# Optimization experiments

Hardware: AMD Instinct MI355X
Metric: run time of the kernel (lower is better)

The kernel has to match this reference:

```python
import jax, jax.numpy as jnp
import numpy as np

B, N, H = 64, 1024, 64
ALPHA = 0.2  # leaky relu negative slope
NEG_BIG = -1.0e12


def setup_inputs() -> dict:
    key = jax.random.key(0)
    k1, k2, k3, k4, k5, k6 = jax.random.split(key, 6)
    inp = jax.random.normal(k1, (B, N, H), dtype=jnp.float32)
    inp_none = jax.random.normal(k2, (B, N, H), dtype=jnp.float32)
    A = (jax.random.uniform(k3, (B, N, N)) < 0.1).astype(jnp.float32)
    # per-sample [i, j] ranges, i <= j < N
    l = jnp.sort(jax.random.randint(k4, (B, 2), 0, N), axis=1)
    # xavier_uniform with gain=1.414 on shape (2H, 1)
    bound = 1.414 * np.sqrt(6.0 / (2 * H + 1))
    a_i = jax.random.uniform(k5, (2 * H, 1), minval=-bound, maxval=bound, dtype=jnp.float32)
    a_c = jax.random.uniform(k6, (2 * H, 1), minval=-bound, maxval=bound, dtype=jnp.float32)
    return {"inp": inp, "inp_none": inp_none, "A": A, "l": l, "a_i": a_i, "a_c": a_c}


def reference(inp, inp_none, A, l, a_i, a_c):
    h = inp.shape[-1]
    n = inp.shape[1]
    # additive-score halves: [B, N, 1]
    Wh1_i = inp_none @ a_i[:h]
    Wh2_i = inp @ a_i[h:]
    Wh1_c = inp @ a_c[:h]
    Wh2_c = inp @ a_c[h:]
    # vectorized replacement of the per-sample range overwrite loop:
    # rows in [l[b,0], l[b,1]) take the a_i branch
    pos = jnp.arange(n)[None, :, None]                       # [1, N, 1]
    in_range = (pos >= l[:, 0, None, None]) & (pos < l[:, 1, None, None])  # [B, N, 1]
    Wh1 = jnp.where(in_range, Wh1_i, Wh1_c)                  # [B, N, 1]
    Wh2 = jnp.where(in_range, Wh2_i, Wh2_c)                  # [B, N, 1]
    # e[b, p, q] = leakyrelu((Wh1[b,p] + Wh2[b,q]) * A[b,p,q])
    e = (Wh1 + jnp.swapaxes(Wh2, 1, 2)) * A                  # [B, N, N]
    e = jnp.where(e >= 0, e, ALPHA * e)
    attn = jnp.where(A > 0, e, NEG_BIG)
    attn = jax.nn.softmax(attn, axis=2)
    h_prime = attn @ inp                                     # [B, N, H]
    return jax.nn.elu(h_prime)  # concat=True
```

## Files before the change

### kernel.cpp

```cpp
#include <hip/hip_runtime.h>
#include <hip/hip_bf16.h>
#include <math.h>
#include <stdint.h>

constexpr int Bn = 64;
constexpr int Nn = 1024;
constexpr int Hn = 64;
constexpr int WAVES = 4;
constexpr int MAXNZ = 256;
constexpr float LRELU_ALPHA = 0.2f;

__device__ __forceinline__ float lrelu(float x) {
    return x >= 0.f ? x : LRELU_ALPHA * x;
}

__global__ __launch_bounds__(256) void wh_kernel(
    const float* __restrict__ inp, const float* __restrict__ inp_none,
    const int* __restrict__ l, const float* __restrict__ a_i,
    const float* __restrict__ a_c,
    float* __restrict__ Wh1, float* __restrict__ Wh2)
{
    const int wave = threadIdx.x >> 6;
    const int lane = threadIdx.x & 63;
    const int row  = blockIdx.x * WAVES + wave;
    const int b    = row >> 10;
    const int n    = row & (Nn - 1);

    const int l0 = l[b * 2], l1 = l[b * 2 + 1];
    const bool in_range = (n >= l0) && (n < l1);

    const size_t base = (size_t)row * Hn + lane;
    const float x1  = in_range ? inp_none[base] : inp[base];
    const float x2  = inp[base];
    const float av1 = in_range ? a_i[lane]      : a_c[lane];
    const float av2 = in_range ? a_i[Hn + lane] : a_c[Hn + lane];

    float p1 = x1 * av1;
    float p2 = x2 * av2;
    #pragma unroll
    for (int off = 32; off > 0; off >>= 1) {
        p1 += __shfl_xor(p1, off);
        p2 += __shfl_xor(p2, off);
    }
    if (lane == 0) {
        Wh1[row] = p1;
        Wh2[row] = p2;
    }
}

__global__ __launch_bounds__(256) void gat_kernel(
    const float* __restrict__ inp, const float* __restrict__ A,
    const float* __restrict__ Wh1, const float* __restrict__ Wh2,
    float* __restrict__ out)
{
    __shared__ float wlds[WAVES][MAXNZ];
    __shared__ int   qlds[WAVES][MAXNZ];

    const int wave = threadIdx.x >> 6;
    const int lane = threadIdx.x & 63;

    const int cpx = gridDim.x >> 3;
    const int bid = blockIdx.x;
    const int swz = (bid & 7) * cpx + (bid >> 3);

    const int row = swz * WAVES + wave;
    const int b   = row >> 10;
    const int p   = row & (Nn - 1);

    const float* __restrict__ Arow = A + ((size_t)b * Nn + p) * Nn;
    const float* __restrict__ Wh2b = Wh2 + b * Nn;
    const float  wh1p = Wh1[b * Nn + p];

    float4 sv[4];
    float  m = -INFINITY;
    #pragma unroll
    for (int k = 0; k < 4; ++k) {
        const int q0 = k * 256 + lane * 4;
        const float4 a4 = *reinterpret_cast<const float4*>(Arow + q0);
        const float4 w2 = *reinterpret_cast<const float4*>(Wh2b + q0);
        float4 s;
        s.x = (a4.x > 0.f) ? lrelu(wh1p + w2.x) : -INFINITY;
        s.y = (a4.y > 0.f) ? lrelu(wh1p + w2.y) : -INFINITY;
        s.z = (a4.z > 0.f) ? lrelu(wh1p + w2.z) : -INFINITY;
        s.w = (a4.w > 0.f) ? lrelu(wh1p + w2.w) : -INFINITY;
        sv[k] = s;
        m = fmaxf(m, fmaxf(fmaxf(s.x, s.y), fmaxf(s.z, s.w)));
    }
    #pragma unroll
    for (int off = 32; off > 0; off >>= 1) m = fmaxf(m, __shfl_xor(m, off));

    const bool empty = (m == -INFINITY);
    const float* __restrict__ inpb = inp + (size_t)b * Nn * Hn;
    float acc0 = 0.f, acc1 = 0.f;

    if (!empty) {
        float4 wv[4];
        float  lsum = 0.f;
        #pragma unroll
        for (int k = 0; k < 4; ++k) {
            float4 s = sv[k];
            float4 w;
            w.x = __expf(s.x - m);
            w.y = __expf(s.y - m);
            w.z = __expf(s.z - m);
            w.w = __expf(s.w - m);
            wv[k] = w;
            lsum += (w.x + w.y) + (w.z + w.w);
        }
        #pragma unroll
        for (int off = 32; off > 0; off >>= 1) lsum += __shfl_xor(lsum, off);
        const float inv = 1.f / lsum;

        int c = 0;
        #pragma unroll
        for (int k = 0; k < 4; ++k) {
            #pragma unroll
            for (int cc = 0; cc < 4; ++cc)
                c += (((const float*)&wv[k])[cc] != 0.f) ? 1 : 0;
        }
        int s = c;
        #pragma unroll
        for (int off = 1; off < 64; off <<= 1) {
            const int t = __shfl_up(s, off);
            if (lane >= off) s += t;
        }
        int j   = s - c;
        int cnt = __shfl(s, 63);

        #pragma unroll
        for (int k = 0; k < 4; ++k) {
            #pragma unroll
            for (int cc = 0; cc < 4; ++cc) {
                const float w = ((const float*)&wv[k])[cc];
                if (w != 0.f && j < MAXNZ) {
                    wlds[wave][j] = w;
                    qlds[wave][j] = (k * 256 + lane * 4 + cc) * Hn;
                    ++j;
                }
            }
        }
        if (cnt > MAXNZ) cnt = MAXNZ;
        asm volatile("s_waitcnt lgkmcnt(0)" ::: "memory");

        int i = 0;
        for (; i + 8 <= cnt; i += 8) {
            const float w0 = wlds[wave][i + 0], w1 = wlds[wave][i + 1];
            const float w2 = wlds[wave][i + 2], w3 = wlds[wave][i + 3];
            const float w4 = wlds[wave][i + 4], w5 = wlds[wave][i + 5];
            const float w6 = wlds[wave][i + 6], w7 = wlds[wave][i + 7];
            const int o0 = qlds[wave][i + 0], o1 = qlds[wave][i + 1];
            const int o2 = qlds[wave][i + 2], o3 = qlds[wave][i + 3];
            const int o4 = qlds[wave][i + 4], o5 = qlds[wave][i + 5];
            const int o6 = qlds[wave][i + 6], o7 = qlds[wave][i + 7];
            const float v0 = inpb[o0 + lane], v1 = inpb[o1 + lane];
            const float v2 = inpb[o2 + lane], v3 = inpb[o3 + lane];
            const float v4 = inpb[o4 + lane], v5 = inpb[o5 + lane];
            const float v6 = inpb[o6 + lane], v7 = inpb[o7 + lane];
            acc0 = fmaf(w0, v0, acc0); acc1 = fmaf(w1, v1, acc1);
            acc0 = fmaf(w2, v2, acc0); acc1 = fmaf(w3, v3, acc1);
            acc0 = fmaf(w4, v4, acc0); acc1 = fmaf(w5, v5, acc1);
            acc0 = fmaf(w6, v6, acc0); acc1 = fmaf(w7, v7, acc1);
        }
        for (; i < cnt; ++i)
            acc0 = fmaf(wlds[wave][i], inpb[qlds[wave][i] + lane], acc0);
        acc0 = (acc0 + acc1) * inv;
    } else {
        for (int q = 0; q < Nn; ++q) acc0 += inpb[q * Hn + lane];
        acc0 *= (1.f / Nn);
    }

    const float r = acc0 > 0.f ? acc0 : expm1f(acc0);
    out[(size_t)row * Hn + lane] = r;
}

extern "C" void kernel_launch(void* const* d_in, const int* in_sizes, int n_in,
                              void* d_out, int out_size, void* d_ws, size_t ws_size,
                              hipStream_t stream) {
    const float* inp      = (const float*)d_in[0];
    const float* inp_none = (const float*)d_in[1];
    const float* A        = (const float*)d_in[2];
    const int*   l        = (const int*)d_in[3];
    const float* a_i      = (const float*)d_in[4];
    const float* a_c      = (const float*)d_in[5];
    float* out = (float*)d_out;

    float* Wh1 = (float*)d_ws;
    float* Wh2 = Wh1 + Bn * Nn;

    const int rows   = Bn * Nn;
    const int blocks = rows / WAVES;

    wh_kernel<<<blocks, 256, 0, stream>>>(inp, inp_none, l, a_i, a_c, Wh1, Wh2);
    gat_kernel<<<blocks, 256, 0, stream>>>(inp, A, Wh1, Wh2, out);
}
```

Before: 472.9 us.

## Replace sparse gather aggregation with tiled bf16 MFMA over transposed inputs

Adds a kernel that converts inp to a transposed bf16 copy. The attention aggregation now processes 32-row tiles per block: it computes unnormalized exp weights into LDS as bf16 and multiplies them against the transposed features with 16x16x32 MFMA instructions. This drops the per-row max pass and the irregular sparse gather, in exchange for dense compute over masked zeros and reduced precision. Skipping max subtraction assumes the scores stay in exp range, and the original per-row kernel remains as a fallback when the workspace is too small.

```diff
diff --git a/kernel.cpp b/kernel.cpp
--- a/kernel.cpp
+++ b/kernel.cpp
@@ -3,16 +3,18 @@
 #include <math.h>
 #include <stdint.h>
 
-constexpr int Bn = 64;
-constexpr int Nn = 1024;
-constexpr int Hn = 64;
-constexpr int WAVES = 4;
-constexpr int MAXNZ = 256;
+constexpr int Bn = 64, Nn = 1024, Hn = 64;
 constexpr float LRELU_ALPHA = 0.2f;
 
-__device__ __forceinline__ float lrelu(float x) {
-    return x >= 0.f ? x : LRELU_ALPHA * x;
-}
+typedef __attribute__((ext_vector_type(8))) short bf16x8;
+typedef __attribute__((ext_vector_type(4))) float f32x4;
+
+__device__ __forceinline__ float lrelu(float x) { return x >= 0.f ? x : LRELU_ALPHA * x; }
+__device__ __forceinline__ ushort f2bf(float x) {
+    uint u = __float_as_uint(x);
+    return (ushort)((u + 0x7FFFu + ((u >> 16) & 1u)) >> 16);
+}
+__device__ __forceinline__ float bf2f(ushort b) { return __uint_as_float(((uint)b) << 16); }
 
 __global__ __launch_bounds__(256) void wh_kernel(
     const float* __restrict__ inp, const float* __restrict__ inp_none,
@@ -22,7 +24,7 @@
 {
     const int wave = threadIdx.x >> 6;
     const int lane = threadIdx.x & 63;
-    const int row  = blockIdx.x * WAVES + wave;
+    const int row  = blockIdx.x * 4 + wave;
     const int b    = row >> 10;
     const int n    = row & (Nn - 1);
 
@@ -48,36 +50,180 @@
     }
 }
 
-__global__ __launch_bounds__(256) void gat_kernel(
+__global__ __launch_bounds__(256) void tconv_kernel(const float* __restrict__ inp,
+                                                    ushort* __restrict__ inpT)
+{
+    __shared__ ushort tile[64][74];
+    const int b  = blockIdx.x >> 4;
+    const int q0 = (blockIdx.x & 15) << 6;
+    const int t  = threadIdx.x;
+    {
+        const int q  = t >> 2;
+        const int h0 = (t & 3) << 4;
+        const float* src = inp + ((size_t)(b * Nn + q0 + q) * Hn + h0);
+        uint* dst = (uint*)&tile[q][h0];
+        #pragma unroll
+        for (int i = 0; i < 4; ++i) {
+            const float4 v = *(const float4*)(src + 4 * i);
+            dst[2 * i + 0] = (uint)f2bf(v.x) | ((uint)f2bf(v.y) << 16);
+            dst[2 * i + 1] = (uint)f2bf(v.z) | ((uint)f2bf(v.w) << 16);
+        }
+    }
+    __syncthreads();
+    {
+        const int h  = t >> 2;
+        const int qb = (t & 3) << 4;
+        uint w[8];
+        #pragma unroll
+        for (int i = 0; i < 8; ++i)
+            w[i] = (uint)tile[qb + 2 * i][h] | ((uint)tile[qb + 2 * i + 1][h] << 16);
+        uint4* dst = (uint4*)(inpT + ((size_t)(b * Hn + h) * Nn + q0 + qb));
+        dst[0] = make_uint4(w[0], w[1], w[2], w[3]);
+        dst[1] = make_uint4(w[4], w[5], w[6], w[7]);
+    }
+}
+
+__global__ __launch_bounds__(256, 4) void gat_mfma_kernel(
+    const float* __restrict__ A, const ushort* __restrict__ inpT,
+    const float* __restrict__ Wh1, const float* __restrict__ Wh2,
+    float* __restrict__ out)
+{
+    __shared__ __align__(16) char pool[18560];
+    float* wh2_lds = (float*)(pool + 16384);
+    float* rs_part = (float*)(pool + 17408);
+    float* inv_lds = (float*)(pool + 18432);
+    float* out_lds = (float*)pool;
+
+    const int t    = threadIdx.x;
+    const int wave = t >> 6;
+    const int lane = t & 63;
+
+    const int d = blockIdx.x;
+    const int o = (d & 7) * 256 + (d >> 3);
+    const int b  = o >> 5;
+    const int p0 = (o & 31) << 5;
+
+    const float*  Ab   = A + (size_t)b * Nn * Nn;
+    const float*  Wh2b = Wh2 + b * Nn;
+    const ushort* Tb   = inpT + (size_t)b * Hn * Nn;
+
+    const int r  = t >> 3;
+    const int qo = (t & 7) << 2;
+    const float wh1_r = Wh1[b * Nn + p0 + r];
+    const float* Arow = Ab + (size_t)(p0 + r) * Nn;
+
+    const int l15 = lane & 15;
+    const int lg  = lane >> 4;
+    const ushort* a_src = Tb + (size_t)(wave * 16 + l15) * Nn + lg * 8;
+    const uint bswz = ((uint)(l15 & 7)) << 4;
+    const uint row0 = (uint)(l15 * 512);
+    const uint row1 = (uint)((l15 + 16) * 512);
+
+    f32x4 acc0 = {0.f, 0.f, 0.f, 0.f};
+    f32x4 acc1 = {0.f, 0.f, 0.f, 0.f};
+    float rs_local = 0.f;
+
+    for (int c = 0; c < 4; ++c) {
+        const int q0 = c * 256;
+        wh2_lds[t] = Wh2b[q0 + t];
+        __syncthreads();
+
+        #pragma unroll
+        for (int j = 0; j < 8; ++j) {
+            const int q = qo + 32 * j;
+            const float4 a4 = *(const float4*)(Arow + q0 + q);
+            const float4 w2 = *(const float4*)(wh2_lds + q);
+            const float s0 = lrelu(wh1_r + w2.x);
+            const float s1 = lrelu(wh1_r + w2.y);
+            const float s2 = lrelu(wh1_r + w2.z);
+            const float s3 = lrelu(wh1_r + w2.w);
+            const ushort u0 = f2bf(a4.x > 0.f ? __expf(s0) : 0.f);
+            const ushort u1 = f2bf(a4.y > 0.f ? __expf(s1) : 0.f);
+            const ushort u2 = f2bf(a4.z > 0.f ? __expf(s2) : 0.f);
+            const ushort u3 = f2bf(a4.w > 0.f ? __expf(s3) : 0.f);
+            rs_local += (bf2f(u0) + bf2f(u1)) + (bf2f(u2) + bf2f(u3));
+            const uint lo = (uint)u0 | ((uint)u1 << 16);
+            const uint hi = (uint)u2 | ((uint)u3 << 16);
+            const uint byte = ((uint)(r * 512 + q * 2)) ^ (((uint)(r & 7)) << 4);
+            *(uint2*)(pool + byte) = make_uint2(lo, hi);
+        }
+        __syncthreads();
+
+        #pragma unroll
+        for (int kk = 0; kk < 8; ++kk) {
+            const uint col = ((uint)(lg * 16 + kk * 64)) ^ bswz;
+            const bf16x8 af = *(const bf16x8*)(a_src + q0 + kk * 32);
+            const bf16x8 b0 = *(const bf16x8*)(pool + (row0 + col));
+            const bf16x8 b1 = *(const bf16x8*)(pool + (row1 + col));
+            acc0 = __builtin_amdgcn_mfma_f32_16x16x32_bf16(af, b0, acc0, 0, 0, 0);
+            acc1 = __builtin_amdgcn_mfma_f32_16x16x32_bf16(af, b1, acc1, 0, 0, 0);
+        }
+        __syncthreads();
+    }
+
+    rs_part[t] = rs_local;
+    __syncthreads();
+    if (t < 32) {
+        float s = 0.f;
+        #pragma unroll
+        for (int j = 0; j < 8; ++j) s += rs_part[t * 8 + j];
+        inv_lds[t] = s > 0.f ? 1.f / s : 0.f;
+    }
+    __syncthreads();
+
+    #pragma unroll
+    for (int nt = 0; nt < 2; ++nt) {
+        const int p = nt * 16 + l15;
+        const float inv = inv_lds[p];
+        const f32x4 a = nt ? acc1 : acc0;
+        #pragma unroll
+        for (int rg = 0; rg < 4; ++rg) {
+            const int h = wave * 16 + lg * 4 + rg;
+            out_lds[p * 65 + h] = a[rg] * inv;
+        }
+    }
+    __syncthreads();
+
+    {
+        const int p  = t >> 3;
+        const int h0 = (t & 7) << 3;
+        float v[8];
+        #pragma unroll
+        for (int i = 0; i < 8; ++i) {
+            const float x = out_lds[p * 65 + h0 + i];
+            v[i] = x > 0.f ? x : expm1f(x);
+        }
+        float* orow = out + (size_t)(b * Nn + p0 + p) * Hn + h0;
+        *(float4*)(orow)     = make_float4(v[0], v[1], v[2], v[3]);
+        *(float4*)(orow + 4) = make_float4(v[4], v[5], v[6], v[7]);
+    }
+}
+
+__global__ __launch_bounds__(256) void gat_fallback_kernel(
     const float* __restrict__ inp, const float* __restrict__ A,
     const float* __restrict__ Wh1, const float* __restrict__ Wh2,
     float* __restrict__ out)
 {
-    __shared__ float wlds[WAVES][MAXNZ];
-    __shared__ int   qlds[WAVES][MAXNZ];
-
+    __shared__ float wlds[4][256];
+    __shared__ int   qlds[4][256];
     const int wave = threadIdx.x >> 6;
     const int lane = threadIdx.x & 63;
-
     const int cpx = gridDim.x >> 3;
     const int bid = blockIdx.x;
     const int swz = (bid & 7) * cpx + (bid >> 3);
-
-    const int row = swz * WAVES + wave;
+    const int row = swz * 4 + wave;
     const int b   = row >> 10;
     const int p   = row & (Nn - 1);
-
-    const float* __restrict__ Arow = A + ((size_t)b * Nn + p) * Nn;
-    const float* __restrict__ Wh2b = Wh2 + b * Nn;
+    const float* Arow = A + ((size_t)b * Nn + p) * Nn;
+    const float* Wh2b = Wh2 + b * Nn;
     const float  wh1p = Wh1[b * Nn + p];
-
     float4 sv[4];
     float  m = -INFINITY;
     #pragma unroll
     for (int k = 0; k < 4; ++k) {
         const int q0 = k * 256 + lane * 4;
-        const float4 a4 = *reinterpret_cast<const float4*>(Arow + q0);
-        const float4 w2 = *reinterpret_cast<const float4*>(Wh2b + q0);
+        const float4 a4 = *(const float4*)(Arow + q0);
+        const float4 w2 = *(const float4*)(Wh2b + q0);
         float4 s;
         s.x = (a4.x > 0.f) ? lrelu(wh1p + w2.x) : -INFINITY;
         s.y = (a4.y > 0.f) ? lrelu(wh1p + w2.y) : -INFINITY;
@@ -88,11 +234,9 @@
     }
     #pragma unroll
     for (int off = 32; off > 0; off >>= 1) m = fmaxf(m, __shfl_xor(m, off));
-
     const bool empty = (m == -INFINITY);
-    const float* __restrict__ inpb = inp + (size_t)b * Nn * Hn;
+    const float* inpb = inp + (size_t)b * Nn * Hn;
     float acc0 = 0.f, acc1 = 0.f;
-
     if (!empty) {
         float4 wv[4];
         float  lsum = 0.f;
@@ -100,66 +244,51 @@
         for (int k = 0; k < 4; ++k) {
             float4 s = sv[k];
             float4 w;
-            w.x = __expf(s.x - m);
-            w.y = __expf(s.y - m);
-            w.z = __expf(s.z - m);
-            w.w = __expf(s.w - m);
+            w.x = __expf(s.x - m); w.y = __expf(s.y - m);
+            w.z = __expf(s.z - m); w.w = __expf(s.w - m);
             wv[k] = w;
             lsum += (w.x + w.y) + (w.z + w.w);
         }
         #pragma unroll
         for (int off = 32; off > 0; off >>= 1) lsum += __shfl_xor(lsum, off);
         const float inv = 1.f / lsum;
-
         int c = 0;
         #pragma unroll
-        for (int k = 0; k < 4; ++k) {
+        for (int k = 0; k < 4; ++k)
             #pragma unroll
             for (int cc = 0; cc < 4; ++cc)
                 c += (((const float*)&wv[k])[cc] != 0.f) ? 1 : 0;
-        }
         int s = c;
         #pragma unroll
         for (int off = 1; off < 64; off <<= 1) {
-            const int t = __shfl_up(s, off);
-            if (lane >= off) s += t;
+            const int tt = __shfl_up(s, off);
+            if (lane >= off) s += tt;
         }
         int j   = s - c;
         int cnt = __shfl(s, 63);
-
-        #pragma unroll
-        for (int k = 0; k < 4; ++k) {
+        #pragma unroll
+        for (int k = 0; k < 4; ++k)
             #pragma unroll
             for (int cc = 0; cc < 4; ++cc) {
                 const float w = ((const float*)&wv[k])[cc];
-                if (w != 0.f && j < MAXNZ) {
+                if (w != 0.f && j < 256) {
                     wlds[wave][j] = w;
                     qlds[wave][j] = (k * 256 + lane * 4 + cc) * Hn;
                     ++j;
                 }
             }
-        }
-        if (cnt > MAXNZ) cnt = MAXNZ;
+        if (cnt > 256) cnt = 256;
         asm volatile("s_waitcnt lgkmcnt(0)" ::: "memory");
-
         int i = 0;
-        for (; i + 8 <= cnt; i += 8) {
-            const float w0 = wlds[wave][i + 0], w1 = wlds[wave][i + 1];
+        for (; i + 4 <= cnt; i += 4) {
+            const float w0 = wlds[wave][i], w1 = wlds[wave][i + 1];
             const float w2 = wlds[wave][i + 2], w3 = wlds[wave][i + 3];
-            const float w4 = wlds[wave][i + 4], w5 = wlds[wave][i + 5];
-            const float w6 = wlds[wave][i + 6], w7 = wlds[wave][i + 7];
-            const int o0 = qlds[wave][i + 0], o1 = qlds[wave][i + 1];
+            const int o0 = qlds[wave][i], o1 = qlds[wave][i + 1];
             const int o2 = qlds[wave][i + 2], o3 = qlds[wave][i + 3];
-            const int o4 = qlds[wave][i + 4], o5 = qlds[wave][i + 5];
-            const int o6 = qlds[wave][i + 6], o7 = qlds[wave][i + 7];
-            const float v0 = inpb[o0 + lane], v1 = inpb[o1 + lane];
-            const float v2 = inpb[o2 + lane], v3 = inpb[o3 + lane];
-            const float v4 = inpb[o4 + lane], v5 = inpb[o5 + lane];
-            const float v6 = inpb[o6 + lane], v7 = inpb[o7 + lane];
-            acc0 = fmaf(w0, v0, acc0); acc1 = fmaf(w1, v1, acc1);
-            acc0 = fmaf(w2, v2, acc0); acc1 = fmaf(w3, v3, acc1);
-            acc0 = fmaf(w4, v4, acc0); acc1 = fmaf(w5, v5, acc1);
-            acc0 = fmaf(w6, v6, acc0); acc1 = fmaf(w7, v7, acc1);
+            acc0 = fmaf(w0, inpb[o0 + lane], acc0);
+            acc1 = fmaf(w1, inpb[o1 + lane], acc1);
+            acc0 = fmaf(w2, inpb[o2 + lane], acc0);
+            acc1 = fmaf(w3, inpb[o3 + lane], acc1);
         }
         for (; i < cnt; ++i)
             acc0 = fmaf(wlds[wave][i], inpb[qlds[wave][i] + lane], acc0);
@@ -168,9 +297,8 @@
         for (int q = 0; q < Nn; ++q) acc0 += inpb[q * Hn + lane];
         acc0 *= (1.f / Nn);
     }
-
-    const float r = acc0 > 0.f ? acc0 : expm1f(acc0);
-    out[(size_t)row * Hn + lane] = r;
+    const float rr = acc0 > 0.f ? acc0 : expm1f(acc0);
+    out[(size_t)row * Hn + lane] = rr;
 }
 
 extern "C" void kernel_launch(void* const* d_in, const int* in_sizes, int n_in,
@@ -184,12 +312,18 @@
     const float* a_c      = (const float*)d_in[5];
     float* out = (float*)d_out;
 
-    float* Wh1 = (float*)d_ws;
-    float* Wh2 = Wh1 + Bn * Nn;
-
-    const int rows   = Bn * Nn;
-    const int blocks = rows / WAVES;
-
-    wh_kernel<<<blocks, 256, 0, stream>>>(inp, inp_none, l, a_i, a_c, Wh1, Wh2);
-    gat_kernel<<<blocks, 256, 0, stream>>>(inp, A, Wh1, Wh2, out);
-}
+    float*  Wh1  = (float*)d_ws;
+    float*  Wh2  = Wh1 + Bn * Nn;
+    ushort* inpT = (ushort*)((char*)d_ws + (size_t)2 * Bn * Nn * 4);
+
+    const size_t need = (size_t)2 * Bn * Nn * 4 + (size_t)Bn * Hn * Nn * 2;
+
+    wh_kernel<<<Bn * Nn / 4, 256, 0, stream>>>(inp, inp_none, l, a_i, a_c, Wh1, Wh2);
+
+    if (ws_size >= need) {
+        tconv_kernel<<<Bn * 16, 256, 0, stream>>>(inp, inpT);
+        gat_mfma_kernel<<<Bn * 32, 256, 0, stream>>>(A, inpT, Wh1, Wh2, out);
+    } else {
+        gat_fallback_kernel<<<Bn * Nn / 4, 256, 0, stream>>>(inp, A, Wh1, Wh2, out);
+    }
+}
```

Result: faster. 425.7 us (-10.0%).
